# Optimization experiments

Measured on AMD Instinct MI355X. Metric: run time of the kernel, lower is better.

The kernel has to match this reference:

```python
import jax, jax.numpy as jnp
import numpy as np


def setup_inputs() -> dict:
    key = jax.random.key(0)
    k1, k2 = jax.random.split(key)
    B, Te, Td, D = 8, 2048, 2048, 256
    encoder_outputs = jax.random.normal(k1, (B, Te, D), dtype=jnp.float32)
    decoder_outputs = jax.random.normal(k2, (B, Td, D), dtype=jnp.float32)
    return {"encoder_outputs": encoder_outputs, "decoder_outputs": decoder_outputs}


def reference(encoder_outputs, decoder_outputs):
    # score[b, e, t] = enc[b, e, :] . dec[b, t, :]   -> [B, Te, Td]
    score = jnp.einsum('bed,btd->bet', encoder_outputs, decoder_outputs)
    # softmax over the encoder-time axis (axis=1), matching K.softmax(..., axis=1)
    attn = jax.nn.softmax(score, axis=1)
    # context[b, t, d] = sum_e attn[b, e, t] * enc[b, e, d]
    # (original does expand_dims + broadcast-mul + sum; einsum is the same math)
    context = jnp.einsum('bet,bed->btd', attn, encoder_outputs)
    return jnp.concatenate([decoder_outputs, context], axis=-1)  # [B, Td, 2D]
```

## Files before the change

kernel.cpp:

```cpp
#include <hip/hip_runtime.h>


#define B_   8
#define TE   2048
#define TD   2048
#define D_   256
#define NIT  32

typedef _Float16 f16x8 __attribute__((ext_vector_type(8)));
typedef float f32x4 __attribute__((ext_vector_type(4)));

__device__ __forceinline__ unsigned pk2(float a, float b) {
  unsigned short ua = __builtin_bit_cast(unsigned short, (_Float16)a);
  unsigned short ub = __builtin_bit_cast(unsigned short, (_Float16)b);
  return (unsigned)ua | ((unsigned)ub << 16);
}

#define GLOAD16(gsrc, ldst)                                                  \
  __builtin_amdgcn_global_load_lds(                                          \
      (const __attribute__((address_space(1))) unsigned int*)(const void*)(gsrc), \
      (__attribute__((address_space(3))) unsigned int*)(void*)(ldst), 16, 0, 0)

__global__ __launch_bounds__(256) void prep_k(const float* __restrict__ enc,
                                              _Float16* __restrict__ out) {
  int idx = blockIdx.x * 256 + threadIdx.x;
  int row = idx >> 5, x = idx & 31;
  int xs = x ^ (row & 7);
  const float* src = enc + (size_t)row * 256 + xs * 8;
  float4 v0 = *(const float4*)src;
  float4 v1 = *(const float4*)(src + 4);
  f16x8 h;
  h[0] = (_Float16)v0.x; h[1] = (_Float16)v0.y; h[2] = (_Float16)v0.z; h[3] = (_Float16)v0.w;
  h[4] = (_Float16)v1.x; h[5] = (_Float16)v1.y; h[6] = (_Float16)v1.z; h[7] = (_Float16)v1.w;
  *(f16x8*)(out + (size_t)idx * 8) = h;
}

__global__ __launch_bounds__(256) void prep_vt(const float* __restrict__ enc,
                                               _Float16* __restrict__ outT) {
  __shared__ float tile[64][65];
  int bid = blockIdx.x;
  int b = bid >> 7, r = bid & 127;
  int et = r >> 2, dt = r & 3;
  int e0 = et * 64, d0 = dt * 64;
  int tx = threadIdx.x & 63, ty = threadIdx.x >> 6;
  const float* src = enc + ((size_t)b * TE + e0) * D_ + d0;
#pragma unroll
  for (int i = 0; i < 16; ++i) {
    int e = i * 4 + ty;
    tile[e][tx] = src[(size_t)e * D_ + tx];
  }
  __syncthreads();
#pragma unroll
  for (int i = 0; i < 16; ++i) {
    int idx = i * 256 + threadIdx.x;
    int d_loc = idx >> 6, eT = idx & 63;
    int d = d0 + d_loc;
    int ctl = eT >> 5, e32 = eT & 31;
    int y = e32 >> 3, j = e32 & 7;
    int ysrc = y ^ ((d >> 1) & 3);
    int esrc = ctl * 32 + ysrc * 8 + j;
    size_t o = (((size_t)b * 64 + (e0 >> 5) + ctl) * 256 + d) * 32 + e32;
    outT[o] = (_Float16)tile[esrc][d_loc];
  }
}

__global__ __launch_bounds__(512, 2) void luong_main(
    const _Float16* __restrict__ encK,
    const _Float16* __restrict__ encVt,
    const float* __restrict__ dec,
    float* __restrict__ out) {
  extern __shared__ char lds[];
  const int tid = threadIdx.x;
  const int lane = tid & 63, wave = tid >> 6;
  const int wr = wave >> 2, wc = wave & 3;
  const int g = lane >> 4, c = lane & 15;

  int bidl = (blockIdx.x & 7) * 32 + (blockIdx.x >> 3);
  const int b = bidl >> 5;
  const int q0 = (bidl & 31) * 64;
  const int t = q0 + wc * 16 + c;

  const float* decB = dec + (size_t)b * TD * D_;
  float* outB = out + (size_t)b * TD * (2 * D_);

  f16x8 qh[8], ql[8];
  {
    const float* qrow = decB + (size_t)t * D_;
#pragma unroll
    for (int dc = 0; dc < 8; ++dc) {
      float4 v0 = *(const float4*)(qrow + dc * 32 + 8 * g);
      float4 v1 = *(const float4*)(qrow + dc * 32 + 8 * g + 4);
      float f[8] = {v0.x, v0.y, v0.z, v0.w, v1.x, v1.y, v1.z, v1.w};
      f16x8 H, L;
#pragma unroll
      for (int j = 0; j < 8; ++j) {
        _Float16 h = (_Float16)f[j];
        H[j] = h;
        L[j] = (_Float16)(f[j] - (float)h);
      }
      qh[dc] = H; ql[dc] = L;
    }
  }

#pragma unroll
  for (int i = 0; i < 8; ++i) {
    int ci = tid + 512 * i;
    int rr = ci >> 6, d4 = (ci & 63) << 2;
    *(float4*)(outB + (size_t)(q0 + rr) * 512 + d4) =
        *(const float4*)(decB + (size_t)(q0 + rr) * 256 + d4);
  }

  const _Float16* kbase = encK + ((size_t)b * TE + wr * 1024) * D_;
  const _Float16* vbase = encVt + ((size_t)b * 64 + wr * 32) * 8192;

  auto STAGE = [&](int buf, int it) {
    char* Kd = lds + (size_t)(buf * 2 + wr) * 32768;
    char* Vd = Kd + 16384;
    const _Float16* ks = kbase + (size_t)it * 8192;
    const _Float16* vs = vbase + (size_t)it * 8192;
#pragma unroll
    for (int q = 0; q < 4; ++q) {
      int chunk = wc * 256 + q * 64 + lane;
      GLOAD16(ks + (size_t)chunk * 8, Kd + wc * 4096 + q * 1024);
      GLOAD16(vs + (size_t)chunk * 8, Vd + wc * 4096 + q * 1024);
    }
  };

  float m_run = -INFINITY, l_run = 0.f;
  f32x4 ctx[16];
#pragma unroll
  for (int i = 0; i < 16; ++i) ctx[i] = (f32x4){0.f, 0.f, 0.f, 0.f};

  STAGE(0, 0);
  __syncthreads();

  for (int it = 0; it < NIT; ++it) {
    int buf = it & 1;
    if (it + 1 < NIT) STAGE(buf ^ 1, it + 1);

    const char* Kb = lds + (size_t)(buf * 2 + wr) * 32768;
    const char* Vb = Kb + 16384;

    f32x4 sA = (f32x4){0.f, 0.f, 0.f, 0.f};
    f32x4 sB = (f32x4){0.f, 0.f, 0.f, 0.f};
    const int e0 = c, e1 = 16 + c;
#pragma unroll
    for (int dc = 0; dc < 8; ++dc) {
      int x = dc * 4 + g;
      f16x8 k0 = *(const f16x8*)(Kb + e0 * 512 + ((x ^ (e0 & 7)) << 4));
      f16x8 k1 = *(const f16x8*)(Kb + e1 * 512 + ((x ^ (e1 & 7)) << 4));
      sA = __builtin_amdgcn_mfma_f32_16x16x32_f16(k0, qh[dc], sA, 0, 0, 0);
      sA = __builtin_amdgcn_mfma_f32_16x16x32_f16(k0, ql[dc], sA, 0, 0, 0);
      sB = __builtin_amdgcn_mfma_f32_16x16x32_f16(k1, qh[dc], sB, 0, 0, 0);
      sB = __builtin_amdgcn_mfma_f32_16x16x32_f16(k1, ql[dc], sB, 0, 0, 0);
    }

    float vmax = fmaxf(fmaxf(fmaxf(sA[0], sA[1]), fmaxf(sA[2], sA[3])),
                       fmaxf(fmaxf(sB[0], sB[1]), fmaxf(sB[2], sB[3])));
    vmax = fmaxf(vmax, __shfl_xor(vmax, 16, 64));
    vmax = fmaxf(vmax, __shfl_xor(vmax, 32, 64));
    float m_new = fmaxf(m_run, vmax);
    float alpha = __expf(m_run - m_new);
    float p0 = __expf(sA[0] - m_new), p1 = __expf(sA[1] - m_new);
    float p2 = __expf(sA[2] - m_new), p3 = __expf(sA[3] - m_new);
    float p4 = __expf(sB[0] - m_new), p5 = __expf(sB[1] - m_new);
    float p6 = __expf(sB[2] - m_new), p7 = __expf(sB[3] - m_new);
    float ps = ((p0 + p1) + (p2 + p3)) + ((p4 + p5) + (p6 + p7));
    ps += __shfl_xor(ps, 16, 64);
    ps += __shfl_xor(ps, 32, 64);
    l_run = l_run * alpha + ps;
    m_run = m_new;
    unsigned w00 = pk2(p0, p1), w10 = pk2(p2, p3);
    unsigned w01 = pk2(p4, p5), w11 = pk2(p6, p7);
#pragma unroll
    for (int i = 0; i < 16; ++i) ctx[i] *= alpha;

    int srcA = (2 * (g & 1)) * 16 + c, srcB = srcA + 16;
    int y0 = __shfl((int)w00, srcA, 64), y1 = __shfl((int)w10, srcA, 64);
    int y2 = __shfl((int)w00, srcB, 64), y3 = __shfl((int)w10, srcB, 64);
    int z0 = __shfl((int)w01, srcA, 64), z1 = __shfl((int)w11, srcA, 64);
    int z2 = __shfl((int)w01, srcB, 64), z3 = __shfl((int)w11, srcB, 64);
    int4 bi = (g >> 1) ? make_int4(z0, z1, z2, z3) : make_int4(y0, y1, y2, y3);
    f16x8 bfrag = __builtin_bit_cast(f16x8, bi);

#pragma unroll
    for (int dt = 0; dt < 16; ++dt) {
      int row = dt * 16 + c;
      f16x8 af = *(const f16x8*)(Vb + row * 64 + ((g ^ ((row >> 1) & 3)) << 4));
      ctx[dt] = __builtin_amdgcn_mfma_f32_16x16x32_f16(af, bfrag, ctx[dt], 0, 0, 0);
    }
    __syncthreads();
  }

  float* mlb = (float*)(lds + 69632);
  if (lane < 16) {
    mlb[((wr * 4 + wc) * 16 + c) * 2 + 0] = m_run;
    mlb[((wr * 4 + wc) * 16 + c) * 2 + 1] = l_run;
  }
  __syncthreads();
  float m_o = mlb[(((1 - wr) * 4 + wc) * 16 + c) * 2 + 0];
  float l_o = mlb[(((1 - wr) * 4 + wc) * 16 + c) * 2 + 1];
  float M = fmaxf(m_run, m_o);
  float fme = __expf(m_run - M);
  float L = l_run * fme + l_o * __expf(m_o - M);
  float invL = 1.0f / L;

  float* Xb = (float*)lds + wc * 4352;
  if (wr == 1) {
#pragma unroll
    for (int dt = 0; dt < 16; ++dt)
#pragma unroll
      for (int r = 0; r < 4; ++r) {
        int d = dt * 16 + 4 * g + r;
        Xb[d * 17 + c] = ctx[dt][r] * fme;
      }
  }
  __syncthreads();
  if (wr == 0) {
    float* orow = outB + (size_t)t * 512 + 256;
#pragma unroll
    for (int dt = 0; dt < 16; ++dt) {
      float4 v;
      float vv[4];
#pragma unroll
      for (int r = 0; r < 4; ++r) {
        int d = dt * 16 + 4 * g + r;
        vv[r] = (ctx[dt][r] * fme + Xb[d * 17 + c]) * invL;
      }
      v.x = vv[0]; v.y = vv[1]; v.z = vv[2]; v.w = vv[3];
      *(float4*)(orow + dt * 16 + 4 * g) = v;
    }
  }
}

extern "C" void kernel_launch(void* const* d_in, const int* in_sizes, int n_in,
                              void* d_out, int out_size, void* d_ws, size_t ws_size,
                              hipStream_t stream) {
  const float* enc = (const float*)d_in[0];
  const float* dec = (const float*)d_in[1];
  float* out = (float*)d_out;
  (void)in_sizes; (void)n_in; (void)out_size; (void)ws_size;

  _Float16* encK  = (_Float16*)d_ws;
  _Float16* encVt = (_Float16*)((char*)d_ws + 8388608);

  prep_k<<<2048, 256, 0, stream>>>(enc, encK);
  prep_vt<<<1024, 256, 0, stream>>>(enc, encVt);
  luong_main<<<256, 512, 131072, stream>>>(encK, encVt, dec, out);
}
```

Measured before the change: 153.8 us.

## Fuse prep kernels, software-pipeline QK with PV, and add lazy softmax rescaling

The two fp16 preprocessing kernels become one that reads each encoder tile once and writes both the K layout and the transposed V layout as 16-byte stores. The main loop is software-pipelined: QK for the next tile runs alongside PV for the current tile under raised wave priority, with the staging order adjusted to match. Online-softmax rescaling of the context is skipped unless the block max grows by more than 8. The decoder copy now runs while the first tile loads. These changes cut launches, global traffic and per-iteration VALU work, but the lazy rescale can let exponentials reach about e^8 before rounding to fp16, and the extra live registers could hurt occupancy.

```diff
diff --git a/kernel.cpp b/kernel.cpp
--- a/kernel.cpp
+++ b/kernel.cpp
@@ -21,22 +21,9 @@
       (const __attribute__((address_space(1))) unsigned int*)(const void*)(gsrc), \
       (__attribute__((address_space(3))) unsigned int*)(void*)(ldst), 16, 0, 0)
 
-__global__ __launch_bounds__(256) void prep_k(const float* __restrict__ enc,
-                                              _Float16* __restrict__ out) {
-  int idx = blockIdx.x * 256 + threadIdx.x;
-  int row = idx >> 5, x = idx & 31;
-  int xs = x ^ (row & 7);
-  const float* src = enc + (size_t)row * 256 + xs * 8;
-  float4 v0 = *(const float4*)src;
-  float4 v1 = *(const float4*)(src + 4);
-  f16x8 h;
-  h[0] = (_Float16)v0.x; h[1] = (_Float16)v0.y; h[2] = (_Float16)v0.z; h[3] = (_Float16)v0.w;
-  h[4] = (_Float16)v1.x; h[5] = (_Float16)v1.y; h[6] = (_Float16)v1.z; h[7] = (_Float16)v1.w;
-  *(f16x8*)(out + (size_t)idx * 8) = h;
-}
-
-__global__ __launch_bounds__(256) void prep_vt(const float* __restrict__ enc,
-                                               _Float16* __restrict__ outT) {
+__global__ __launch_bounds__(256) void prep_fused(const float* __restrict__ enc,
+                                                  _Float16* __restrict__ encK,
+                                                  _Float16* __restrict__ encVt) {
   __shared__ float tile[64][65];
   int bid = blockIdx.x;
   int b = bid >> 7, r = bid & 127;
@@ -45,22 +32,33 @@
   int tx = threadIdx.x & 63, ty = threadIdx.x >> 6;
   const float* src = enc + ((size_t)b * TE + e0) * D_ + d0;
 #pragma unroll
-  for (int i = 0; i < 16; ++i) {
-    int e = i * 4 + ty;
-    tile[e][tx] = src[(size_t)e * D_ + tx];
-  }
-  __syncthreads();
-#pragma unroll
-  for (int i = 0; i < 16; ++i) {
-    int idx = i * 256 + threadIdx.x;
-    int d_loc = idx >> 6, eT = idx & 63;
-    int d = d0 + d_loc;
-    int ctl = eT >> 5, e32 = eT & 31;
-    int y = e32 >> 3, j = e32 & 7;
-    int ysrc = y ^ ((d >> 1) & 3);
-    int esrc = ctl * 32 + ysrc * 8 + j;
-    size_t o = (((size_t)b * 64 + (e0 >> 5) + ctl) * 256 + d) * 32 + e32;
-    outT[o] = (_Float16)tile[esrc][d_loc];
+  for (int i = 0; i < 16; ++i)
+    tile[i * 4 + ty][tx] = src[(size_t)(i * 4 + ty) * D_ + tx];
+  __syncthreads();
+
+  _Float16* kout = encK + ((size_t)b * TE + e0) * D_ + d0;
+#pragma unroll
+  for (int i = 0; i < 2; ++i) {
+    int ci = i * 256 + threadIdx.x;
+    int e = ci >> 3, xl = ci & 7;
+    int xs = xl ^ (e & 7);
+    const float* s8 = &tile[e][xs * 8];
+    f16x8 h;
+#pragma unroll
+    for (int j = 0; j < 8; ++j) h[j] = (_Float16)s8[j];
+    *(f16x8*)(kout + (size_t)e * D_ + xl * 8) = h;
+  }
+#pragma unroll
+  for (int i = 0; i < 2; ++i) {
+    int u = i * 256 + threadIdx.x;
+    int y = u & 3, d_loc = (u >> 2) & 63, ctl = u >> 8;
+    int s = (d_loc >> 1) & 3;
+    int ebase = ctl * 32 + ((y ^ s) << 3);
+    f16x8 h;
+#pragma unroll
+    for (int j = 0; j < 8; ++j) h[j] = (_Float16)tile[ebase + j][d_loc];
+    size_t o = (((size_t)b * 64 + et * 2 + ctl) * 256 + d0 + d_loc) * 32 + y * 8;
+    *(f16x8*)(encVt + o) = h;
   }
 }
 
@@ -102,14 +100,6 @@
     }
   }
 
-#pragma unroll
-  for (int i = 0; i < 8; ++i) {
-    int ci = tid + 512 * i;
-    int rr = ci >> 6, d4 = (ci & 63) << 2;
-    *(float4*)(outB + (size_t)(q0 + rr) * 512 + d4) =
-        *(const float4*)(decB + (size_t)(q0 + rr) * 256 + d4);
-  }
-
   const _Float16* kbase = encK + ((size_t)b * TE + wr * 1024) * D_;
   const _Float16* vbase = encVt + ((size_t)b * 64 + wr * 32) * 8192;
 
@@ -131,65 +121,98 @@
 #pragma unroll
   for (int i = 0; i < 16; ++i) ctx[i] = (f32x4){0.f, 0.f, 0.f, 0.f};
 
-  STAGE(0, 0);
-  __syncthreads();
-
-  for (int it = 0; it < NIT; ++it) {
-    int buf = it & 1;
-    if (it + 1 < NIT) STAGE(buf ^ 1, it + 1);
-
-    const char* Kb = lds + (size_t)(buf * 2 + wr) * 32768;
-    const char* Vb = Kb + 16384;
-
-    f32x4 sA = (f32x4){0.f, 0.f, 0.f, 0.f};
-    f32x4 sB = (f32x4){0.f, 0.f, 0.f, 0.f};
-    const int e0 = c, e1 = 16 + c;
+  f32x4 sA, sB;
+  f16x8 bfrag;
+
+  auto QK = [&](const char* Kb, f32x4& oA, f32x4& oB) {
+    oA = (f32x4){0.f, 0.f, 0.f, 0.f};
+    oB = (f32x4){0.f, 0.f, 0.f, 0.f};
+    const int el0 = c, el1 = 16 + c;
 #pragma unroll
     for (int dc = 0; dc < 8; ++dc) {
       int x = dc * 4 + g;
-      f16x8 k0 = *(const f16x8*)(Kb + e0 * 512 + ((x ^ (e0 & 7)) << 4));
-      f16x8 k1 = *(const f16x8*)(Kb + e1 * 512 + ((x ^ (e1 & 7)) << 4));
-      sA = __builtin_amdgcn_mfma_f32_16x16x32_f16(k0, qh[dc], sA, 0, 0, 0);
-      sA = __builtin_amdgcn_mfma_f32_16x16x32_f16(k0, ql[dc], sA, 0, 0, 0);
-      sB = __builtin_amdgcn_mfma_f32_16x16x32_f16(k1, qh[dc], sB, 0, 0, 0);
-      sB = __builtin_amdgcn_mfma_f32_16x16x32_f16(k1, ql[dc], sB, 0, 0, 0);
-    }
-
+      int xsw = (x & 24) | ((x ^ el0) & 7);
+      f16x8 k0 = *(const f16x8*)(Kb + el0 * 512 + (xsw << 4));
+      f16x8 k1 = *(const f16x8*)(Kb + el1 * 512 + (xsw << 4));
+      oA = __builtin_amdgcn_mfma_f32_16x16x32_f16(k0, qh[dc], oA, 0, 0, 0);
+      oA = __builtin_amdgcn_mfma_f32_16x16x32_f16(k0, ql[dc], oA, 0, 0, 0);
+      oB = __builtin_amdgcn_mfma_f32_16x16x32_f16(k1, qh[dc], oB, 0, 0, 0);
+      oB = __builtin_amdgcn_mfma_f32_16x16x32_f16(k1, ql[dc], oB, 0, 0, 0);
+    }
+  };
+
+  auto PV = [&](const char* Vb) {
+#pragma unroll
+    for (int dt = 0; dt < 16; ++dt) {
+      int row = dt * 16 + c;
+      f16x8 af = *(const f16x8*)(Vb + row * 64 + ((g ^ ((row >> 1) & 3)) << 4));
+      ctx[dt] = __builtin_amdgcn_mfma_f32_16x16x32_f16(af, bfrag, ctx[dt], 0, 0, 0);
+    }
+  };
+
+  auto SOFTMAX = [&]() {
     float vmax = fmaxf(fmaxf(fmaxf(sA[0], sA[1]), fmaxf(sA[2], sA[3])),
                        fmaxf(fmaxf(sB[0], sB[1]), fmaxf(sB[2], sB[3])));
     vmax = fmaxf(vmax, __shfl_xor(vmax, 16, 64));
     vmax = fmaxf(vmax, __shfl_xor(vmax, 32, 64));
-    float m_new = fmaxf(m_run, vmax);
-    float alpha = __expf(m_run - m_new);
-    float p0 = __expf(sA[0] - m_new), p1 = __expf(sA[1] - m_new);
-    float p2 = __expf(sA[2] - m_new), p3 = __expf(sA[3] - m_new);
-    float p4 = __expf(sB[0] - m_new), p5 = __expf(sB[1] - m_new);
-    float p6 = __expf(sB[2] - m_new), p7 = __expf(sB[3] - m_new);
+    if (!__all(vmax <= m_run + 8.0f)) {
+      float m_new = fmaxf(m_run, vmax);
+      float alpha = __expf(m_run - m_new);
+      l_run *= alpha;
+#pragma unroll
+      for (int i = 0; i < 16; ++i) ctx[i] *= alpha;
+      m_run = m_new;
+    }
+    float p0 = __expf(sA[0] - m_run), p1 = __expf(sA[1] - m_run);
+    float p2 = __expf(sA[2] - m_run), p3 = __expf(sA[3] - m_run);
+    float p4 = __expf(sB[0] - m_run), p5 = __expf(sB[1] - m_run);
+    float p6 = __expf(sB[2] - m_run), p7 = __expf(sB[3] - m_run);
     float ps = ((p0 + p1) + (p2 + p3)) + ((p4 + p5) + (p6 + p7));
     ps += __shfl_xor(ps, 16, 64);
     ps += __shfl_xor(ps, 32, 64);
-    l_run = l_run * alpha + ps;
-    m_run = m_new;
+    l_run += ps;
     unsigned w00 = pk2(p0, p1), w10 = pk2(p2, p3);
     unsigned w01 = pk2(p4, p5), w11 = pk2(p6, p7);
-#pragma unroll
-    for (int i = 0; i < 16; ++i) ctx[i] *= alpha;
-
     int srcA = (2 * (g & 1)) * 16 + c, srcB = srcA + 16;
     int y0 = __shfl((int)w00, srcA, 64), y1 = __shfl((int)w10, srcA, 64);
     int y2 = __shfl((int)w00, srcB, 64), y3 = __shfl((int)w10, srcB, 64);
     int z0 = __shfl((int)w01, srcA, 64), z1 = __shfl((int)w11, srcA, 64);
     int z2 = __shfl((int)w01, srcB, 64), z3 = __shfl((int)w11, srcB, 64);
     int4 bi = (g >> 1) ? make_int4(z0, z1, z2, z3) : make_int4(y0, y1, y2, y3);
-    f16x8 bfrag = __builtin_bit_cast(f16x8, bi);
-
-#pragma unroll
-    for (int dt = 0; dt < 16; ++dt) {
-      int row = dt * 16 + c;
-      f16x8 af = *(const f16x8*)(Vb + row * 64 + ((g ^ ((row >> 1) & 3)) << 4));
-      ctx[dt] = __builtin_amdgcn_mfma_f32_16x16x32_f16(af, bfrag, ctx[dt], 0, 0, 0);
-    }
+    bfrag = __builtin_bit_cast(f16x8, bi);
+  };
+
+  STAGE(0, 0);
+#pragma unroll
+  for (int i = 0; i < 8; ++i) {
+    int ci = tid + 512 * i;
+    int rr = ci >> 6, d4 = (ci & 63) << 2;
+    *(float4*)(outB + (size_t)(q0 + rr) * 512 + d4) =
+        *(const float4*)(decB + (size_t)(q0 + rr) * 256 + d4);
+  }
+  __syncthreads();
+  STAGE(1, 1);
+  QK(lds + (size_t)wr * 32768, sA, sB);
+  SOFTMAX();
+  __syncthreads();
+
+#pragma unroll 2
+  for (int it = 0; it < NIT; ++it) {
+    const int cur = it & 1;
+    const char* bufC = lds + (size_t)(cur * 2 + wr) * 32768;
+    const char* bufN = lds + (size_t)((cur ^ 1) * 2 + wr) * 32768;
+    f32x4 nA, nB;
+    __builtin_amdgcn_s_setprio(1);
+    if (it + 1 < NIT) QK(bufN, nA, nB);
+    PV(bufC + 16384);
+    __builtin_amdgcn_s_setprio(0);
     __syncthreads();
+    if (it + 2 < NIT) STAGE(cur, it + 2);
+    if (it + 1 < NIT) {
+      sA = nA; sB = nB;
+      SOFTMAX();
+      __syncthreads();
+    }
   }
 
   float* mlb = (float*)(lds + 69632);
@@ -244,7 +267,6 @@
   _Float16* encK  = (_Float16*)d_ws;
   _Float16* encVt = (_Float16*)((char*)d_ws + 8388608);
 
-  prep_k<<<2048, 256, 0, stream>>>(enc, encK);
-  prep_vt<<<1024, 256, 0, stream>>>(enc, encVt);
+  prep_fused<<<1024, 256, 0, stream>>>(enc, encK, encVt);
   luong_main<<<256, 512, 131072, stream>>>(encK, encVt, dec, out);
 }
```

Result: slower. 165.4 us (+7.5%).
